# Kernel optimization log

Measured on AMD Instinct MI355X. Metric: run time of the kernel, lower is better.

Reference implementation:

```python
import jax, jax.numpy as jnp
import numpy as np

NEG_SLOPE = 0.2
STRONG_CONVEXITY = 0.5


def _scalar(x, Wq, Wl, bl, Wz, wz_out, wq_out, wl_out):
    # x: [B, D]; Wq/Wl: [L, H, D]; bl: [L, H]; Wz: [L-1, H, H]
    # Precompute all per-layer x-dependent terms in two batched einsums.
    qx = jnp.einsum('lhd,bd->lbh', Wq, x) ** 2          # [L, B, H]
    lx = jnp.einsum('lhd,bd->lbh', Wl, x) + bl[:, None, :]  # [L, B, H]
    z = jax.nn.leaky_relu(qx[0] + lx[0], negative_slope=NEG_SLOPE)

    def step(z, inputs):
        W, q, l = inputs
        z = jax.nn.leaky_relu(z @ W.T + q + l, negative_slope=NEG_SLOPE)
        return z, None

    z, _ = jax.lax.scan(step, z, (Wz, qx[1:], lx[1:]))
    # Final layer to scalar output (no bias on last wx_lin per torch code).
    out = z @ wz_out.T + (x @ wq_out.T) ** 2 + x @ wl_out.T  # [B, 1]
    return out


def setup_inputs() -> dict:
    key = jax.random.key(0)
    ks = jax.random.split(key, 8)
    B, D, H, L = 8192, 128, 512, 10
    f32 = jnp.float32
    x = jax.random.normal(ks[0], (B, D), f32)
    Wq = jax.random.normal(ks[1], (L, H, D), f32) * (1.0 / np.sqrt(D))
    Wl = jax.random.normal(ks[2], (L, H, D), f32) * (1.0 / np.sqrt(D))
    bl = jax.random.normal(ks[3], (L, H), f32) * 0.01
    # wz weights are kept non-negative in the original (clamp/exp init)
    Wz = jnp.abs(jax.random.normal(ks[4], (L - 1, H, H), f32)) * (1.0 / np.sqrt(H))
    wz_out = jnp.abs(jax.random.normal(ks[5], (1, H), f32)) * (1.0 / np.sqrt(H))
    wq_out = jax.random.normal(ks[6], (1, D), f32) * (1.0 / np.sqrt(D))
    wl_out = jax.random.normal(ks[7], (1, D), f32) * (1.0 / np.sqrt(D))
    return {"x": x, "Wq": Wq, "Wl": Wl, "bl": bl, "Wz": Wz,
            "wz_out": wz_out, "wq_out": wq_out, "wl_out": wl_out}


def reference(x, Wq, Wl, bl, Wz, wz_out, wq_out, wl_out):
    # forward = (1 - mu) * d(scalar)/dx + mu * x, with grad_outputs = ones
    def scalar_sum(xx):
        return jnp.sum(_scalar(xx, Wq, Wl, bl, Wz, wz_out, wq_out, wl_out))

    gx = jax.grad(scalar_sum)(x)  # per-sample gradient, [B, D]
    return (1.0 - STRONG_CONVEXITY) * gx + STRONG_CONVEXITY * x
```

## Files before the change

kernel.cpp:

```cpp
#include <hip/hip_runtime.h>


#define Bn 8192
#define Dn 128
#define Hn 512
#define Ln 10

constexpr float NS = 0.2f;

typedef __attribute__((ext_vector_type(8))) short short8;
typedef __attribute__((ext_vector_type(4))) float f32x4;

typedef const __attribute__((address_space(1))) void GV;
typedef __attribute__((address_space(3))) void LV;

__device__ __forceinline__ void gload16(const void* g, void* l) {
    __builtin_amdgcn_global_load_lds((GV*)g, (LV*)l, 16, 0, 0);
}

#define MFMA(acc, a, b) acc = __builtin_amdgcn_mfma_f32_16x16x32_bf16(a, b, acc, 0, 0, 0)

__device__ __forceinline__ unsigned short bf16_rne(float v) {
    unsigned u = __float_as_uint(v);
    u += 0x7FFFu + ((u >> 16) & 1u);
    return (unsigned short)(u >> 16);
}
__device__ __forceinline__ float bf2f(unsigned short h) {
    return __uint_as_float(((unsigned)h) << 16);
}
__device__ __forceinline__ void split2(float v, unsigned short& h, unsigned short& l) {
    h = bf16_rne(v);
    l = bf16_rne(v - bf2f(h));
}


__global__ __launch_bounds__(256) void split_flat(const float* __restrict__ in,
        unsigned short* __restrict__ hi, unsigned short* __restrict__ lo, int n4) {
    int i = blockIdx.x * 256 + threadIdx.x;
    if (i >= n4) return;
    float4 v = ((const float4*)in)[i];
    ushort4 h, l;
    split2(v.x, h.x, l.x);
    split2(v.y, h.y, l.y);
    split2(v.z, h.z, l.z);
    split2(v.w, h.w, l.w);
    ((ushort4*)hi)[i] = h;
    ((ushort4*)lo)[i] = l;
}

__global__ __launch_bounds__(256) void split_both(const float* __restrict__ in,
        unsigned short* __restrict__ hi, unsigned short* __restrict__ lo,
        unsigned short* __restrict__ thi, unsigned short* __restrict__ tlo,
        int R, int C) {
    __shared__ float t[32][33];
    const size_t off = (size_t)blockIdx.z * R * C;
    const float* src = in + off;
    unsigned short* sh_ = hi + off;
    unsigned short* sl_ = lo + off;
    unsigned short* dh = thi + off;
    unsigned short* dl = tlo + off;
    const int r0 = blockIdx.x * 32, c0 = blockIdx.y * 32;
    const int tr = threadIdx.x >> 5, tc = threadIdx.x & 31;
#pragma unroll
    for (int i = 0; i < 4; ++i) {
        size_t si = (size_t)(r0 + tr + 8 * i) * C + c0 + tc;
        float v = src[si];
        t[tr + 8 * i][tc] = v;
        unsigned short h, l; split2(v, h, l);
        sh_[si] = h; sl_[si] = l;
    }
    __syncthreads();
#pragma unroll
    for (int i = 0; i < 4; ++i) {
        float v = t[tc][tr + 8 * i];
        unsigned short h, l; split2(v, h, l);
        size_t o = (size_t)(c0 + tr + 8 * i) * R + r0 + tc;
        dh[o] = h; dl[o] = l;
    }
}


__global__ __launch_bounds__(256) void fwd_mfma(
    const unsigned short* __restrict__ xh, const unsigned short* __restrict__ xl,
    const unsigned short* __restrict__ zph, const unsigned short* __restrict__ zpl,
    const unsigned short* __restrict__ Wzh, const unsigned short* __restrict__ Wzl,
    const unsigned short* __restrict__ Wqh, const unsigned short* __restrict__ Wql,
    const unsigned short* __restrict__ Wlh, const unsigned short* __restrict__ Wll,
    const float* __restrict__ bl,
    unsigned short* __restrict__ zoh, unsigned short* __restrict__ zol,
    unsigned short* __restrict__ mask16, float* __restrict__ uout, int hasZ)
{
    __shared__ __align__(16) char smem[32768];
    unsigned short* Ah  = (unsigned short*)smem;
    unsigned short* Al  = (unsigned short*)(smem + 8192);
    unsigned short* B0h = (unsigned short*)(smem + 16384);
    unsigned short* B0l = (unsigned short*)(smem + 20480);
    unsigned short* B1h = (unsigned short*)(smem + 24576);
    unsigned short* B1l = (unsigned short*)(smem + 28672);

    const int tid = threadIdx.x;
    const int w = tid >> 6, lane = tid & 63;
    const int lq = lane >> 4, lc = lane & 15;
    const int wm = (w & 1) * 64, wn = (w >> 1) * 32;
    const int row0 = blockIdx.x * 128, col0 = blockIdx.y * 64;
    const int sr = lane >> 2, sk = (lane & 3) * 8;

    f32x4 accz[4][2], accu[4][2], accv[4][2];
#pragma unroll
    for (int i = 0; i < 4; ++i)
#pragma unroll
        for (int j = 0; j < 2; ++j)
#pragma unroll
            for (int r = 0; r < 4; ++r) { accz[i][j][r] = 0.f; accu[i][j][r] = 0.f; accv[i][j][r] = 0.f; }

    if (hasZ) {
        for (int k0 = 0; k0 < Hn; k0 += 32) {
            __syncthreads();
            for (int c = w; c < 8; c += 4) {
                size_t go = (size_t)(row0 + c * 16 + sr) * Hn + k0 + sk;
                gload16(zph + go, Ah + c * 512);
                gload16(zpl + go, Al + c * 512);
            }
            {
                int c = w;
                size_t go = (size_t)(col0 + c * 16 + sr) * Hn + k0 + sk;
                gload16(Wzh + go, B0h + c * 512);
                gload16(Wzl + go, B0l + c * 512);
            }
            __syncthreads();
            short8 ah[4], al[4];
#pragma unroll
            for (int mt = 0; mt < 4; ++mt) {
                int ao = (wm + mt * 16 + lc) * 32 + lq * 8;
                ah[mt] = *(const short8*)(Ah + ao);
                al[mt] = *(const short8*)(Al + ao);
            }
#pragma unroll
            for (int nt = 0; nt < 2; ++nt) {
                int bo = (wn + nt * 16 + lc) * 32 + lq * 8;
                short8 bh = *(const short8*)(B0h + bo);
                short8 bv = *(const short8*)(B0l + bo);
#pragma unroll
                for (int mt = 0; mt < 4; ++mt) {
                    MFMA(accz[mt][nt], ah[mt], bh);
                    MFMA(accz[mt][nt], ah[mt], bv);
                    MFMA(accz[mt][nt], al[mt], bh);
                }
            }
        }
    }

    for (int k0 = 0; k0 < Dn; k0 += 32) {
        __syncthreads();
        for (int c = w; c < 8; c += 4) {
            size_t go = (size_t)(row0 + c * 16 + sr) * Dn + k0 + sk;
            gload16(xh + go, Ah + c * 512);
            gload16(xl + go, Al + c * 512);
        }
        {
            int c = w;
            size_t go = (size_t)(col0 + c * 16 + sr) * Dn + k0 + sk;
            gload16(Wqh + go, B0h + c * 512);
            gload16(Wql + go, B0l + c * 512);
            gload16(Wlh + go, B1h + c * 512);
            gload16(Wll + go, B1l + c * 512);
        }
        __syncthreads();
        short8 ah[4], al[4];
#pragma unroll
        for (int mt = 0; mt < 4; ++mt) {
            int ao = (wm + mt * 16 + lc) * 32 + lq * 8;
            ah[mt] = *(const short8*)(Ah + ao);
            al[mt] = *(const short8*)(Al + ao);
        }
#pragma unroll
        for (int nt = 0; nt < 2; ++nt) {
            int bo = (wn + nt * 16 + lc) * 32 + lq * 8;
            short8 bqh = *(const short8*)(B0h + bo);
            short8 bql = *(const short8*)(B0l + bo);
            short8 blh = *(const short8*)(B1h + bo);
            short8 bll = *(const short8*)(B1l + bo);
#pragma unroll
            for (int mt = 0; mt < 4; ++mt) {
                MFMA(accu[mt][nt], ah[mt], bqh);
                MFMA(accu[mt][nt], ah[mt], bql);
                MFMA(accu[mt][nt], al[mt], bqh);
                MFMA(accv[mt][nt], ah[mt], blh);
                MFMA(accv[mt][nt], ah[mt], bll);
                MFMA(accv[mt][nt], al[mt], blh);
            }
        }
    }

#pragma unroll
    for (int nt = 0; nt < 2; ++nt) {
        const int colb = col0 + wn + nt * 16;
        const int col = colb + lc;
        const float blv = bl[col];
#pragma unroll
        for (int mt = 0; mt < 4; ++mt) {
            const int rowb = row0 + wm + mt * 16;
#pragma unroll
            for (int r = 0; r < 4; ++r) {
                float uq = accu[mt][nt][r];
                float pre = accz[mt][nt][r] + uq * uq + accv[mt][nt][r] + blv;
                bool m = pre >= 0.f;
                unsigned long long bal = __ballot(m);
                if (lc == 0) {
                    int rw = rowb + lq * 4 + r;
                    mask16[(size_t)rw * 32 + (colb >> 4)] =
                        (unsigned short)((bal >> (lq * 16)) & 0xFFFFull);
                }
                float zv = m ? pre : NS * pre;
                unsigned short h, l; split2(zv, h, l);
                size_t o = (size_t)(rowb + lq * 4 + r) * Hn + col;
                zoh[o] = h; zol[o] = l;
                uout[o] = uq;
            }
        }
    }
}


__global__ __launch_bounds__(256) void bwd_combo(
    const unsigned short* __restrict__ gah, const unsigned short* __restrict__ gal,
    const unsigned short* __restrict__ WzTh, const unsigned short* __restrict__ WzTl,
    const unsigned short* __restrict__ maskprev,
    unsigned short* __restrict__ goh, unsigned short* __restrict__ gol,
    const float* __restrict__ uL,
    const unsigned short* __restrict__ WqTh, const unsigned short* __restrict__ WqTl,
    const unsigned short* __restrict__ WlTh, const unsigned short* __restrict__ WlTl,
    float* __restrict__ gx, int addTo, int nG, int finalF,
    const float* __restrict__ xin, const float* __restrict__ s,
    const float* __restrict__ wq_out, const float* __restrict__ wl_out)
{
    __shared__ __align__(16) char smem[49152];
    const int bid = blockIdx.x;
    const int tid = threadIdx.x;
    const int w = tid >> 6, lane = tid & 63;
    const int lq = lane >> 4, lc = lane & 15;
    const int wm = (w & 1) * 64, wn = (w >> 1) * 32;
    const int sr = lane >> 2, sk = (lane & 3) * 8;

    if (bid < nG) {
        unsigned short* Ah  = (unsigned short*)smem;
        unsigned short* Al  = (unsigned short*)(smem + 8192);
        unsigned short* B0h = (unsigned short*)(smem + 16384);
        unsigned short* B0l = (unsigned short*)(smem + 20480);
        const int row0 = (bid & 63) * 128, col0 = (bid >> 6) * 64;

        f32x4 acc[4][2];
#pragma unroll
        for (int i = 0; i < 4; ++i)
#pragma unroll
            for (int j = 0; j < 2; ++j)
#pragma unroll
                for (int r = 0; r < 4; ++r) acc[i][j][r] = 0.f;

        for (int k0 = 0; k0 < Hn; k0 += 32) {
            __syncthreads();
            for (int c = w; c < 8; c += 4) {
                size_t go = (size_t)(row0 + c * 16 + sr) * Hn + k0 + sk;
                gload16(gah + go, Ah + c * 512);
                gload16(gal + go, Al + c * 512);
            }
            {
                int c = w;
                size_t go = (size_t)(col0 + c * 16 + sr) * Hn + k0 + sk;
                gload16(WzTh + go, B0h + c * 512);
                gload16(WzTl + go, B0l + c * 512);
            }
            __syncthreads();
            short8 ah[4], al[4];
#pragma unroll
            for (int mt = 0; mt < 4; ++mt) {
                int ao = (wm + mt * 16 + lc) * 32 + lq * 8;
                ah[mt] = *(const short8*)(Ah + ao);
                al[mt] = *(const short8*)(Al + ao);
            }
#pragma unroll
            for (int nt = 0; nt < 2; ++nt) {
                int bo = (wn + nt * 16 + lc) * 32 + lq * 8;
                short8 bh = *(const short8*)(B0h + bo);
                short8 bv = *(const short8*)(B0l + bo);
#pragma unroll
                for (int mt = 0; mt < 4; ++mt) {
                    MFMA(acc[mt][nt], ah[mt], bh);
                    MFMA(acc[mt][nt], ah[mt], bv);
                    MFMA(acc[mt][nt], al[mt], bh);
                }
            }
        }

#pragma unroll
        for (int nt = 0; nt < 2; ++nt) {
            const int colb = col0 + wn + nt * 16;
            const int col = colb + lc;
#pragma unroll
            for (int mt = 0; mt < 4; ++mt) {
                const int rowb = row0 + wm + mt * 16;
#pragma unroll
                for (int r = 0; r < 4; ++r) {
                    int row = rowb + lq * 4 + r;
                    unsigned short wbits = maskprev[(size_t)row * 32 + (colb >> 4)];
                    float f = ((wbits >> lc) & 1) ? 1.f : NS;
                    float v = acc[mt][nt][r] * f;
                    unsigned short h, l; split2(v, h, l);
                    size_t o = (size_t)row * Hn + col;
                    goh[o] = h; gol[o] = l;
                }
            }
        }
    } else {
        unsigned short* A1h = (unsigned short*)smem;
        unsigned short* A1l = (unsigned short*)(smem + 8192);
        unsigned short* A2h = (unsigned short*)(smem + 16384);
        unsigned short* A2l = (unsigned short*)(smem + 24576);
        unsigned short* Bqh = (unsigned short*)(smem + 32768);
        unsigned short* Bql = (unsigned short*)(smem + 36864);
        unsigned short* Blh = (unsigned short*)(smem + 40960);
        unsigned short* Bll = (unsigned short*)(smem + 45056);

        const int t = bid - nG;
        const int row0 = (t >> 1) * 128, col0 = (t & 1) * 64;
        const int ar = tid >> 2, as = (tid & 3) * 8;

        f32x4 acc[4][2];
#pragma unroll
        for (int i = 0; i < 4; ++i)
#pragma unroll
            for (int j = 0; j < 2; ++j)
#pragma unroll
                for (int r = 0; r < 4; ++r) acc[i][j][r] = 0.f;

        for (int k0 = 0; k0 < Hn; k0 += 32) {
            __syncthreads();
            {
                int c = w;
                size_t go = (size_t)(col0 + c * 16 + sr) * Hn + k0 + sk;
                gload16(WqTh + go, Bqh + c * 512);
                gload16(WqTl + go, Bql + c * 512);
                gload16(WlTh + go, Blh + c * 512);
                gload16(WlTl + go, Bll + c * 512);
            }
#pragma unroll
            for (int rr = 0; rr < 2; ++rr) {
                const int lr = rr * 64 + ar;
                size_t gb = (size_t)(row0 + lr) * Hn + k0 + as;
                float4 u0 = *(const float4*)(uL + gb);
                float4 u1 = *(const float4*)(uL + gb + 4);
                ushort4 h0 = *(const ushort4*)(gah + gb);
                ushort4 h1 = *(const ushort4*)(gah + gb + 4);
                ushort4 l0 = *(const ushort4*)(gal + gb);
                ushort4 l1 = *(const ushort4*)(gal + gb + 4);
                int lo_ = lr * 32 + as;
                *(ushort4*)(A2h + lo_) = h0; *(ushort4*)(A2h + lo_ + 4) = h1;
                *(ushort4*)(A2l + lo_) = l0; *(ushort4*)(A2l + lo_ + 4) = l1;
                ushort4 oh, ol;
                float g, a1;
                g = bf2f(h0.x) + bf2f(l0.x); a1 = 2.f * u0.x * g; split2(a1, oh.x, ol.x);
                g = bf2f(h0.y) + bf2f(l0.y); a1 = 2.f * u0.y * g; split2(a1, oh.y, ol.y);
                g = bf2f(h0.z) + bf2f(l0.z); a1 = 2.f * u0.z * g; split2(a1, oh.z, ol.z);
                g = bf2f(h0.w) + bf2f(l0.w); a1 = 2.f * u0.w * g; split2(a1, oh.w, ol.w);
                *(ushort4*)(A1h + lo_) = oh; *(ushort4*)(A1l + lo_) = ol;
                g = bf2f(h1.x) + bf2f(l1.x); a1 = 2.f * u1.x * g; split2(a1, oh.x, ol.x);
                g = bf2f(h1.y) + bf2f(l1.y); a1 = 2.f * u1.y * g; split2(a1, oh.y, ol.y);
                g = bf2f(h1.z) + bf2f(l1.z); a1 = 2.f * u1.z * g; split2(a1, oh.z, ol.z);
                g = bf2f(h1.w) + bf2f(l1.w); a1 = 2.f * u1.w * g; split2(a1, oh.w, ol.w);
                *(ushort4*)(A1h + lo_ + 4) = oh; *(ushort4*)(A1l + lo_ + 4) = ol;
            }
            __syncthreads();
            short8 a1h[4], a1l[4], a2h[4], a2l[4];
#pragma unroll
            for (int mt = 0; mt < 4; ++mt) {
                int ao = (wm + mt * 16 + lc) * 32 + lq * 8;
                a1h[mt] = *(const short8*)(A1h + ao);
                a1l[mt] = *(const short8*)(A1l + ao);
                a2h[mt] = *(const short8*)(A2h + ao);
                a2l[mt] = *(const short8*)(A2l + ao);
            }
#pragma unroll
            for (int nt = 0; nt < 2; ++nt) {
                int bo = (wn + nt * 16 + lc) * 32 + lq * 8;
                short8 qh = *(const short8*)(Bqh + bo);
                short8 ql_ = *(const short8*)(Bql + bo);
                short8 lh = *(const short8*)(Blh + bo);
                short8 ll_ = *(const short8*)(Bll + bo);
#pragma unroll
                for (int mt = 0; mt < 4; ++mt) {
                    MFMA(acc[mt][nt], a1h[mt], qh);
                    MFMA(acc[mt][nt], a1h[mt], ql_);
                    MFMA(acc[mt][nt], a1l[mt], qh);
                    MFMA(acc[mt][nt], a2h[mt], lh);
                    MFMA(acc[mt][nt], a2h[mt], ll_);
                    MFMA(acc[mt][nt], a2l[mt], lh);
                }
            }
        }

#pragma unroll
        for (int nt = 0; nt < 2; ++nt) {
            const int col = col0 + wn + nt * 16 + lc;
#pragma unroll
            for (int mt = 0; mt < 4; ++mt) {
                const int rowb = row0 + wm + mt * 16;
#pragma unroll
                for (int r = 0; r < 4; ++r) {
                    const int row = rowb + lq * 4 + r;
                    size_t o = (size_t)row * Dn + col;
                    float v = acc[mt][nt][r];
                    if (addTo) v += gx[o];
                    if (finalF) {
                        v = 0.5f * v + s[row] * wq_out[col] + 0.5f * wl_out[col]
                            + 0.5f * xin[o];
                    }
                    gx[o] = v;
                }
            }
        }
    }
}


__global__ __launch_bounds__(256) void ga_init(
    const float* __restrict__ wz_out, const unsigned short* __restrict__ mask9,
    unsigned short* __restrict__ gh, unsigned short* __restrict__ gl)
{
    int i = blockIdx.x * 256 + threadIdx.x;
    int e = i << 2;
    int b = e >> 9, h = e & 511;
    unsigned short wbits = mask9[(size_t)b * 32 + (h >> 4)];
    float4 wv = *(const float4*)(wz_out + h);
    int sh = h & 15;
    ushort4 oh, ol;
    float f;
    f = wv.x * (((wbits >> (sh + 0)) & 1) ? 1.f : NS); split2(f, oh.x, ol.x);
    f = wv.y * (((wbits >> (sh + 1)) & 1) ? 1.f : NS); split2(f, oh.y, ol.y);
    f = wv.z * (((wbits >> (sh + 2)) & 1) ? 1.f : NS); split2(f, oh.z, ol.z);
    f = wv.w * (((wbits >> (sh + 3)) & 1) ? 1.f : NS); split2(f, oh.w, ol.w);
    *(ushort4*)(gh + e) = oh;
    *(ushort4*)(gl + e) = ol;
}

__global__ __launch_bounds__(256) void rowdot_kernel(
    const float* __restrict__ x, const float* __restrict__ wq_out, float* __restrict__ s) {
    const int b = blockIdx.x * 4 + (threadIdx.x >> 6);
    const int lane = threadIdx.x & 63;
    float v = x[(size_t)b * Dn + lane] * wq_out[lane] +
              x[(size_t)b * Dn + 64 + lane] * wq_out[64 + lane];
#pragma unroll
    for (int off = 32; off > 0; off >>= 1) v += __shfl_down(v, off, 64);
    if (lane == 0) s[b] = v;
}


extern "C" void kernel_launch(void* const* d_in, const int* in_sizes, int n_in,
                              void* d_out, int out_size, void* d_ws, size_t ws_size,
                              hipStream_t stream) {
    (void)in_sizes; (void)n_in; (void)out_size; (void)ws_size;
    const float* x      = (const float*)d_in[0];
    const float* Wq     = (const float*)d_in[1];
    const float* Wl     = (const float*)d_in[2];
    const float* bl     = (const float*)d_in[3];
    const float* Wz     = (const float*)d_in[4];
    const float* wz_out = (const float*)d_in[5];
    const float* wq_out = (const float*)d_in[6];
    const float* wl_out = (const float*)d_in[7];
    float* out = (float*)d_out;

    char* p = (char*)d_ws;
    #define CARVE(name, bytes) unsigned short* name = (unsigned short*)p; p += (((size_t)(bytes)) + 255) & ~(size_t)255;
    CARVE(xh,  (size_t)Bn*Dn*2)  CARVE(xl,  (size_t)Bn*Dn*2)
    CARVE(Wqh, (size_t)Ln*Hn*Dn*2) CARVE(Wql, (size_t)Ln*Hn*Dn*2)
    CARVE(Wlh, (size_t)Ln*Hn*Dn*2) CARVE(Wll, (size_t)Ln*Hn*Dn*2)
    CARVE(WqTh,(size_t)Ln*Hn*Dn*2) CARVE(WqTl,(size_t)Ln*Hn*Dn*2)
    CARVE(WlTh,(size_t)Ln*Hn*Dn*2) CARVE(WlTl,(size_t)Ln*Hn*Dn*2)
    CARVE(Wzh, (size_t)(Ln-1)*Hn*Hn*2) CARVE(Wzl, (size_t)(Ln-1)*Hn*Hn*2)
    CARVE(WzTh,(size_t)(Ln-1)*Hn*Hn*2) CARVE(WzTl,(size_t)(Ln-1)*Hn*Hn*2)
    CARVE(zAh, (size_t)Bn*Hn*2) CARVE(zAl, (size_t)Bn*Hn*2)
    CARVE(zBh, (size_t)Bn*Hn*2) CARVE(zBl, (size_t)Bn*Hn*2)
    float* uBuf = (float*)p; p += (size_t)Ln*Bn*Hn*4;
    float* s    = (float*)p; p += (size_t)Bn*4;
    unsigned short* mask16 = (unsigned short*)p; p += (size_t)Ln*Bn*32*2;
    #undef CARVE

    split_flat<<<(Bn*Dn/4 + 255)/256, 256, 0, stream>>>(x, xh, xl, Bn*Dn/4);
    split_both<<<dim3(Hn/32, Dn/32, Ln), 256, 0, stream>>>(Wq, Wqh, Wql, WqTh, WqTl, Hn, Dn);
    split_both<<<dim3(Hn/32, Dn/32, Ln), 256, 0, stream>>>(Wl, Wlh, Wll, WlTh, WlTl, Hn, Dn);
    split_both<<<dim3(Hn/32, Hn/32, Ln-1), 256, 0, stream>>>(Wz, Wzh, Wzl, WzTh, WzTl, Hn, Hn);

    rowdot_kernel<<<Bn/4, 256, 0, stream>>>(x, wq_out, s);

    const dim3 gF(Bn/128, Hn/64);

    fwd_mfma<<<gF, 256, 0, stream>>>(xh, xl, nullptr, nullptr, nullptr, nullptr,
        Wqh, Wql, Wlh, Wll, bl, zAh, zAl, mask16, uBuf, 0);
    for (int l = 1; l < Ln; ++l) {
        const unsigned short* zh  = (l & 1) ? zAh : zBh;
        const unsigned short* zl_ = (l & 1) ? zAl : zBl;
        unsigned short* oh  = (l & 1) ? zBh : zAh;
        unsigned short* ol_ = (l & 1) ? zBl : zAl;
        fwd_mfma<<<gF, 256, 0, stream>>>(xh, xl, zh, zl_,
            Wzh + (size_t)(l-1)*Hn*Hn, Wzl + (size_t)(l-1)*Hn*Hn,
            Wqh + (size_t)l*Hn*Dn, Wql + (size_t)l*Hn*Dn,
            Wlh + (size_t)l*Hn*Dn, Wll + (size_t)l*Hn*Dn,
            bl + (size_t)l*Hn, oh, ol_, mask16 + (size_t)l*Bn*32,
            uBuf + (size_t)l*Bn*Hn, 1);
    }

    ga_init<<<(Bn*Hn/4)/256, 256, 0, stream>>>(wz_out, mask16 + (size_t)9*Bn*32, zAh, zAl);
    for (int l = Ln - 1; l >= 0; --l) {
        int sidx = (Ln - 1 - l) & 1;
        const unsigned short* gh_ = sidx ? zBh : zAh;
        const unsigned short* gl_ = sidx ? zBl : zAl;
        unsigned short* oh  = sidx ? zAh : zBh;
        unsigned short* ol_ = sidx ? zAl : zBl;
        const int nG = (l > 0) ? 512 : 0;
        bwd_combo<<<nG + 128, 256, 0, stream>>>(
            gh_, gl_,
            (l > 0) ? WzTh + (size_t)(l-1)*Hn*Hn : nullptr,
            (l > 0) ? WzTl + (size_t)(l-1)*Hn*Hn : nullptr,
            (l > 0) ? mask16 + (size_t)(l-1)*Bn*32 : nullptr,
            (l > 0) ? oh : nullptr, (l > 0) ? ol_ : nullptr,
            uBuf + (size_t)l*Bn*Hn,
            WqTh + (size_t)l*Dn*Hn, WqTl + (size_t)l*Dn*Hn,
            WlTh + (size_t)l*Dn*Hn, WlTl + (size_t)l*Dn*Hn,
            out, (l == Ln - 1) ? 0 : 1, nG, (l == 0) ? 1 : 0,
            x, s, wq_out, wl_out);
    }
}
```

Baseline: 889.7 us.

## Precompute quadratic-branch gradient in producer epilogues and split x-grad tiles smaller

The forward pass now stores the squared-branch pre-activation u as a bf16 hi/lo pair instead of fp32. The backward gradient epilogue, and ga_init for the last layer, then compute a1 = 2*u*g in place for the next layer, so the x-gradient blocks no longer read u and build a1 in shared memory themselves. The x-gradient blocks become a plain two-pass bf16x3 GEMM over 64-row tiles fed by global_load_lds, with half the shared memory and twice as many blocks. The cost is extra read-modify-write traffic in the gradient epilogue, and u is kept only at split-bf16 precision.

```diff
diff --git a/kernel.cpp b/kernel.cpp
--- a/kernel.cpp
+++ b/kernel.cpp
@@ -88,7 +88,8 @@
     const unsigned short* __restrict__ Wlh, const unsigned short* __restrict__ Wll,
     const float* __restrict__ bl,
     unsigned short* __restrict__ zoh, unsigned short* __restrict__ zol,
-    unsigned short* __restrict__ mask16, float* __restrict__ uout, int hasZ)
+    unsigned short* __restrict__ mask16,
+    unsigned short* __restrict__ uoh, unsigned short* __restrict__ uol, int hasZ)
 {
     __shared__ __align__(16) char smem[32768];
     unsigned short* Ah  = (unsigned short*)smem;
@@ -215,7 +216,8 @@
                 unsigned short h, l; split2(zv, h, l);
                 size_t o = (size_t)(rowb + lq * 4 + r) * Hn + col;
                 zoh[o] = h; zol[o] = l;
-                uout[o] = uq;
+                unsigned short uhh, ull; split2(uq, uhh, ull);
+                uoh[o] = uhh; uol[o] = ull;
             }
         }
     }
@@ -227,19 +229,19 @@
     const unsigned short* __restrict__ WzTh, const unsigned short* __restrict__ WzTl,
     const unsigned short* __restrict__ maskprev,
     unsigned short* __restrict__ goh, unsigned short* __restrict__ gol,
-    const float* __restrict__ uL,
+    unsigned short* uph, unsigned short* upl,
+    const unsigned short* __restrict__ a1h_, const unsigned short* __restrict__ a1l_,
     const unsigned short* __restrict__ WqTh, const unsigned short* __restrict__ WqTl,
     const unsigned short* __restrict__ WlTh, const unsigned short* __restrict__ WlTl,
     float* __restrict__ gx, int addTo, int nG, int finalF,
     const float* __restrict__ xin, const float* __restrict__ s,
     const float* __restrict__ wq_out, const float* __restrict__ wl_out)
 {
-    __shared__ __align__(16) char smem[49152];
+    __shared__ __align__(16) char smem[24576];
     const int bid = blockIdx.x;
     const int tid = threadIdx.x;
     const int w = tid >> 6, lane = tid & 63;
     const int lq = lane >> 4, lc = lane & 15;
-    const int wm = (w & 1) * 64, wn = (w >> 1) * 32;
     const int sr = lane >> 2, sk = (lane & 3) * 8;
 
     if (bid < nG) {
@@ -247,6 +249,7 @@
         unsigned short* Al  = (unsigned short*)(smem + 8192);
         unsigned short* B0h = (unsigned short*)(smem + 16384);
         unsigned short* B0l = (unsigned short*)(smem + 20480);
+        const int wm = (w & 1) * 64, wn = (w >> 1) * 32;
         const int row0 = (bid & 63) * 128, col0 = (bid >> 6) * 64;
 
         f32x4 acc[4][2];
@@ -308,92 +311,66 @@
                     unsigned short h, l; split2(v, h, l);
                     size_t o = (size_t)row * Hn + col;
                     goh[o] = h; gol[o] = l;
+                    float uv = bf2f(uph[o]) + bf2f(upl[o]);
+                    float a1v = 2.f * uv * v;
+                    unsigned short h2, l2; split2(a1v, h2, l2);
+                    uph[o] = h2; upl[o] = l2;
                 }
             }
         }
     } else {
-        unsigned short* A1h = (unsigned short*)smem;
-        unsigned short* A1l = (unsigned short*)(smem + 8192);
-        unsigned short* A2h = (unsigned short*)(smem + 16384);
-        unsigned short* A2l = (unsigned short*)(smem + 24576);
-        unsigned short* Bqh = (unsigned short*)(smem + 32768);
-        unsigned short* Bql = (unsigned short*)(smem + 36864);
-        unsigned short* Blh = (unsigned short*)(smem + 40960);
-        unsigned short* Bll = (unsigned short*)(smem + 45056);
-
+        unsigned short* Ah = (unsigned short*)smem;
+        unsigned short* Al = (unsigned short*)(smem + 4096);
+        unsigned short* Bh = (unsigned short*)(smem + 8192);
+        unsigned short* Bl = (unsigned short*)(smem + 12288);
+        const int wm = (w & 1) * 32, wn = (w >> 1) * 32;
         const int t = bid - nG;
-        const int row0 = (t >> 1) * 128, col0 = (t & 1) * 64;
-        const int ar = tid >> 2, as = (tid & 3) * 8;
-
-        f32x4 acc[4][2];
-#pragma unroll
-        for (int i = 0; i < 4; ++i)
+        const int row0 = (t >> 1) * 64, col0 = (t & 1) * 64;
+
+        f32x4 acc[2][2];
+#pragma unroll
+        for (int i = 0; i < 2; ++i)
 #pragma unroll
             for (int j = 0; j < 2; ++j)
 #pragma unroll
                 for (int r = 0; r < 4; ++r) acc[i][j][r] = 0.f;
 
-        for (int k0 = 0; k0 < Hn; k0 += 32) {
-            __syncthreads();
-            {
-                int c = w;
-                size_t go = (size_t)(col0 + c * 16 + sr) * Hn + k0 + sk;
-                gload16(WqTh + go, Bqh + c * 512);
-                gload16(WqTl + go, Bql + c * 512);
-                gload16(WlTh + go, Blh + c * 512);
-                gload16(WlTl + go, Bll + c * 512);
-            }
-#pragma unroll
-            for (int rr = 0; rr < 2; ++rr) {
-                const int lr = rr * 64 + ar;
-                size_t gb = (size_t)(row0 + lr) * Hn + k0 + as;
-                float4 u0 = *(const float4*)(uL + gb);
-                float4 u1 = *(const float4*)(uL + gb + 4);
-                ushort4 h0 = *(const ushort4*)(gah + gb);
-                ushort4 h1 = *(const ushort4*)(gah + gb + 4);
-                ushort4 l0 = *(const ushort4*)(gal + gb);
-                ushort4 l1 = *(const ushort4*)(gal + gb + 4);
-                int lo_ = lr * 32 + as;
-                *(ushort4*)(A2h + lo_) = h0; *(ushort4*)(A2h + lo_ + 4) = h1;
-                *(ushort4*)(A2l + lo_) = l0; *(ushort4*)(A2l + lo_ + 4) = l1;
-                ushort4 oh, ol;
-                float g, a1;
-                g = bf2f(h0.x) + bf2f(l0.x); a1 = 2.f * u0.x * g; split2(a1, oh.x, ol.x);
-                g = bf2f(h0.y) + bf2f(l0.y); a1 = 2.f * u0.y * g; split2(a1, oh.y, ol.y);
-                g = bf2f(h0.z) + bf2f(l0.z); a1 = 2.f * u0.z * g; split2(a1, oh.z, ol.z);
-                g = bf2f(h0.w) + bf2f(l0.w); a1 = 2.f * u0.w * g; split2(a1, oh.w, ol.w);
-                *(ushort4*)(A1h + lo_) = oh; *(ushort4*)(A1l + lo_) = ol;
-                g = bf2f(h1.x) + bf2f(l1.x); a1 = 2.f * u1.x * g; split2(a1, oh.x, ol.x);
-                g = bf2f(h1.y) + bf2f(l1.y); a1 = 2.f * u1.y * g; split2(a1, oh.y, ol.y);
-                g = bf2f(h1.z) + bf2f(l1.z); a1 = 2.f * u1.z * g; split2(a1, oh.z, ol.z);
-                g = bf2f(h1.w) + bf2f(l1.w); a1 = 2.f * u1.w * g; split2(a1, oh.w, ol.w);
-                *(ushort4*)(A1h + lo_ + 4) = oh; *(ushort4*)(A1l + lo_ + 4) = ol;
-            }
-            __syncthreads();
-            short8 a1h[4], a1l[4], a2h[4], a2l[4];
-#pragma unroll
-            for (int mt = 0; mt < 4; ++mt) {
-                int ao = (wm + mt * 16 + lc) * 32 + lq * 8;
-                a1h[mt] = *(const short8*)(A1h + ao);
-                a1l[mt] = *(const short8*)(A1l + ao);
-                a2h[mt] = *(const short8*)(A2h + ao);
-                a2l[mt] = *(const short8*)(A2l + ao);
-            }
-#pragma unroll
-            for (int nt = 0; nt < 2; ++nt) {
-                int bo = (wn + nt * 16 + lc) * 32 + lq * 8;
-                short8 qh = *(const short8*)(Bqh + bo);
-                short8 ql_ = *(const short8*)(Bql + bo);
-                short8 lh = *(const short8*)(Blh + bo);
-                short8 ll_ = *(const short8*)(Bll + bo);
-#pragma unroll
-                for (int mt = 0; mt < 4; ++mt) {
-                    MFMA(acc[mt][nt], a1h[mt], qh);
-                    MFMA(acc[mt][nt], a1h[mt], ql_);
-                    MFMA(acc[mt][nt], a1l[mt], qh);
-                    MFMA(acc[mt][nt], a2h[mt], lh);
-                    MFMA(acc[mt][nt], a2h[mt], ll_);
-                    MFMA(acc[mt][nt], a2l[mt], lh);
+#pragma unroll
+        for (int pass = 0; pass < 2; ++pass) {
+            const unsigned short* Ash = pass ? gah : a1h_;
+            const unsigned short* Asl = pass ? gal : a1l_;
+            const unsigned short* Bsh = pass ? WlTh : WqTh;
+            const unsigned short* Bsl = pass ? WlTl : WqTl;
+            for (int k0 = 0; k0 < Hn; k0 += 32) {
+                __syncthreads();
+                {
+                    int c = w;
+                    size_t ga_ = (size_t)(row0 + c * 16 + sr) * Hn + k0 + sk;
+                    gload16(Ash + ga_, Ah + c * 512);
+                    gload16(Asl + ga_, Al + c * 512);
+                    size_t gb_ = (size_t)(col0 + c * 16 + sr) * Hn + k0 + sk;
+                    gload16(Bsh + gb_, Bh + c * 512);
+                    gload16(Bsl + gb_, Bl + c * 512);
+                }
+                __syncthreads();
+                short8 ah[2], al[2];
+#pragma unroll
+                for (int mt = 0; mt < 2; ++mt) {
+                    int ao = (wm + mt * 16 + lc) * 32 + lq * 8;
+                    ah[mt] = *(const short8*)(Ah + ao);
+                    al[mt] = *(const short8*)(Al + ao);
+                }
+#pragma unroll
+                for (int nt = 0; nt < 2; ++nt) {
+                    int bo = (wn + nt * 16 + lc) * 32 + lq * 8;
+                    short8 bh = *(const short8*)(Bh + bo);
+                    short8 bv = *(const short8*)(Bl + bo);
+#pragma unroll
+                    for (int mt = 0; mt < 2; ++mt) {
+                        MFMA(acc[mt][nt], ah[mt], bh);
+                        MFMA(acc[mt][nt], ah[mt], bv);
+                        MFMA(acc[mt][nt], al[mt], bh);
+                    }
                 }
             }
         }
@@ -402,7 +379,7 @@
         for (int nt = 0; nt < 2; ++nt) {
             const int col = col0 + wn + nt * 16 + lc;
 #pragma unroll
-            for (int mt = 0; mt < 4; ++mt) {
+            for (int mt = 0; mt < 2; ++mt) {
                 const int rowb = row0 + wm + mt * 16;
 #pragma unroll
                 for (int r = 0; r < 4; ++r) {
@@ -424,6 +401,7 @@
 
 __global__ __launch_bounds__(256) void ga_init(
     const float* __restrict__ wz_out, const unsigned short* __restrict__ mask9,
+    unsigned short* uh, unsigned short* ul,
     unsigned short* __restrict__ gh, unsigned short* __restrict__ gl)
 {
     int i = blockIdx.x * 256 + threadIdx.x;
@@ -431,15 +409,23 @@
     int b = e >> 9, h = e & 511;
     unsigned short wbits = mask9[(size_t)b * 32 + (h >> 4)];
     float4 wv = *(const float4*)(wz_out + h);
+    ushort4 u4h = *(const ushort4*)(uh + e);
+    ushort4 u4l = *(const ushort4*)(ul + e);
     int sh = h & 15;
-    ushort4 oh, ol;
-    float f;
+    ushort4 oh, ol, qh, ql;
+    float f, a;
     f = wv.x * (((wbits >> (sh + 0)) & 1) ? 1.f : NS); split2(f, oh.x, ol.x);
+    a = 2.f * (bf2f(u4h.x) + bf2f(u4l.x)) * f; split2(a, qh.x, ql.x);
     f = wv.y * (((wbits >> (sh + 1)) & 1) ? 1.f : NS); split2(f, oh.y, ol.y);
+    a = 2.f * (bf2f(u4h.y) + bf2f(u4l.y)) * f; split2(a, qh.y, ql.y);
     f = wv.z * (((wbits >> (sh + 2)) & 1) ? 1.f : NS); split2(f, oh.z, ol.z);
+    a = 2.f * (bf2f(u4h.z) + bf2f(u4l.z)) * f; split2(a, qh.z, ql.z);
     f = wv.w * (((wbits >> (sh + 3)) & 1) ? 1.f : NS); split2(f, oh.w, ol.w);
+    a = 2.f * (bf2f(u4h.w) + bf2f(u4l.w)) * f; split2(a, qh.w, ql.w);
     *(ushort4*)(gh + e) = oh;
     *(ushort4*)(gl + e) = ol;
+    *(ushort4*)(uh + e) = qh;
+    *(ushort4*)(ul + e) = ql;
 }
 
 __global__ __launch_bounds__(256) void rowdot_kernel(
@@ -479,8 +465,8 @@
     CARVE(WzTh,(size_t)(Ln-1)*Hn*Hn*2) CARVE(WzTl,(size_t)(Ln-1)*Hn*Hn*2)
     CARVE(zAh, (size_t)Bn*Hn*2) CARVE(zAl, (size_t)Bn*Hn*2)
     CARVE(zBh, (size_t)Bn*Hn*2) CARVE(zBl, (size_t)Bn*Hn*2)
-    float* uBuf = (float*)p; p += (size_t)Ln*Bn*Hn*4;
-    float* s    = (float*)p; p += (size_t)Bn*4;
+    CARVE(uLh, (size_t)Ln*Bn*Hn*2) CARVE(uLl, (size_t)Ln*Bn*Hn*2)
+    float* s = (float*)p; p += (size_t)Bn*4;
     unsigned short* mask16 = (unsigned short*)p; p += (size_t)Ln*Bn*32*2;
     #undef CARVE
 
@@ -494,7 +480,7 @@
     const dim3 gF(Bn/128, Hn/64);
 
     fwd_mfma<<<gF, 256, 0, stream>>>(xh, xl, nullptr, nullptr, nullptr, nullptr,
-        Wqh, Wql, Wlh, Wll, bl, zAh, zAl, mask16, uBuf, 0);
+        Wqh, Wql, Wlh, Wll, bl, zAh, zAl, mask16, uLh, uLl, 0);
     for (int l = 1; l < Ln; ++l) {
         const unsigned short* zh  = (l & 1) ? zAh : zBh;
         const unsigned short* zl_ = (l & 1) ? zAl : zBl;
@@ -505,24 +491,27 @@
             Wqh + (size_t)l*Hn*Dn, Wql + (size_t)l*Hn*Dn,
             Wlh + (size_t)l*Hn*Dn, Wll + (size_t)l*Hn*Dn,
             bl + (size_t)l*Hn, oh, ol_, mask16 + (size_t)l*Bn*32,
-            uBuf + (size_t)l*Bn*Hn, 1);
-    }
-
-    ga_init<<<(Bn*Hn/4)/256, 256, 0, stream>>>(wz_out, mask16 + (size_t)9*Bn*32, zAh, zAl);
+            uLh + (size_t)l*Bn*Hn, uLl + (size_t)l*Bn*Hn, 1);
+    }
+
+    ga_init<<<(Bn*Hn/4)/256, 256, 0, stream>>>(wz_out, mask16 + (size_t)9*Bn*32,
+        uLh + (size_t)9*Bn*Hn, uLl + (size_t)9*Bn*Hn, zAh, zAl);
     for (int l = Ln - 1; l >= 0; --l) {
         int sidx = (Ln - 1 - l) & 1;
-        const unsigned short* gh_ = sidx ? zBh : zAh;
-        const unsigned short* gl_ = sidx ? zBl : zAl;
-        unsigned short* oh  = sidx ? zAh : zBh;
-        unsigned short* ol_ = sidx ? zAl : zBl;
+        const unsigned short* gh_  = sidx ? zBh : zAh;
+        const unsigned short* gl_  = sidx ? zBl : zAl;
+        unsigned short* oh   = sidx ? zAh : zBh;
+        unsigned short* ol_  = sidx ? zAl : zBl;
         const int nG = (l > 0) ? 512 : 0;
-        bwd_combo<<<nG + 128, 256, 0, stream>>>(
+        bwd_combo<<<nG + 256, 256, 0, stream>>>(
             gh_, gl_,
             (l > 0) ? WzTh + (size_t)(l-1)*Hn*Hn : nullptr,
             (l > 0) ? WzTl + (size_t)(l-1)*Hn*Hn : nullptr,
             (l > 0) ? mask16 + (size_t)(l-1)*Bn*32 : nullptr,
             (l > 0) ? oh : nullptr, (l > 0) ? ol_ : nullptr,
-            uBuf + (size_t)l*Bn*Hn,
+            (l > 0) ? uLh + (size_t)(l-1)*Bn*Hn : nullptr,
+            (l > 0) ? uLl + (size_t)(l-1)*Bn*Hn : nullptr,
+            uLh + (size_t)l*Bn*Hn, uLl + (size_t)l*Bn*Hn,
             WqTh + (size_t)l*Dn*Hn, WqTl + (size_t)l*Dn*Hn,
             WlTh + (size_t)l*Dn*Hn, WlTl + (size_t)l*Dn*Hn,
             out, (l == Ln - 1) ? 0 : 1, nG, (l == 0) ? 1 : 0,
```

After: 868.3 us. -2.4%, faster.
